# Optimization experiments

Measured on AMD Instinct MI355X. Metric: run time of the kernel, lower is better.

Reference implementation:

```python
import jax, jax.numpy as jnp
import numpy as np

VIS_DIM, VIS_NUM, EMBED, HIDDEN, VOCAB = 512, 196, 256, 512, 10000
B, T = 128, 20


def setup_inputs() -> dict:
    key = jax.random.key(0)
    ks = jax.random.split(key, 16)
    s = 0.02
    return {
        "features": jax.random.normal(ks[0], (B, VIS_NUM, VIS_DIM), jnp.float32),
        "captions": jax.random.randint(ks[1], (B, T), 0, VOCAB),
        "W_init_h": jax.random.normal(ks[2], (HIDDEN, VIS_DIM), jnp.float32) * s,
        "W_init_c": jax.random.normal(ks[3], (HIDDEN, VIS_DIM), jnp.float32) * s,
        "Wv": jax.random.normal(ks[4], (1, VIS_DIM), jnp.float32) * s,
        "bv": jnp.zeros((1,), jnp.float32),
        "Wa": jax.random.normal(ks[5], (1, HIDDEN), jnp.float32) * s,
        "ba": jnp.zeros((1,), jnp.float32),
        "embed_table": jax.random.normal(ks[6], (VOCAB, EMBED), jnp.float32) * s,
        "W_ih": jax.random.normal(ks[7], (4 * HIDDEN, VIS_DIM + EMBED), jnp.float32) * s,
        "W_hh": jax.random.normal(ks[8], (4 * HIDDEN, HIDDEN), jnp.float32) * s,
        "b_ih": jnp.zeros((4 * HIDDEN,), jnp.float32),
        "b_hh": jnp.zeros((4 * HIDDEN,), jnp.float32),
        "Wo": jax.random.normal(ks[9], (VOCAB, HIDDEN), jnp.float32) * s,
        "bo": jnp.zeros((VOCAB,), jnp.float32),
    }


def reference(features, captions, W_init_h, W_init_c, Wv, bv, Wa, ba,
              embed_table, W_ih, W_hh, b_ih, b_hh, Wo, bo):
    b, t = captions.shape
    vis_num = features.shape[1]
    # _init_hidden: sum over spatial locations of a bias-free linear, / vis_num
    h0 = jnp.sum(jnp.einsum('bnv,hv->bnh', features, W_init_h), axis=1) / vis_num  # [B,H]
    c0 = jnp.sum(jnp.einsum('bnv,hv->bnh', features, W_init_c), axis=1) / vis_num  # [B,H]
    emb = embed_table[captions]  # [B,T,E]
    # visual part of attention logits is constant across timesteps
    att_v = jnp.einsum('bnv,ov->bno', features, Wv) + bv  # [B,N,1]

    def step(carry, emb_t):
        h, c = carry
        att = att_v + (h @ Wa.T + ba)[:, None, :]          # [B,N,1]
        alpha = jax.nn.softmax(att, axis=1)                # softmax over vis_num
        ctx = jnp.sum(features * alpha, axis=1)            # [B,vis_dim]
        x = jnp.concatenate([ctx, emb_t], axis=1)          # [B,vis_dim+E]
        gates = x @ W_ih.T + b_ih + h @ W_hh.T + b_hh      # [B,4H]
        i, f, g, o = jnp.split(gates, 4, axis=1)           # torch LSTM gate order
        i, f, o = jax.nn.sigmoid(i), jax.nn.sigmoid(f), jax.nn.sigmoid(o)
        g = jnp.tanh(g)
        c = f * c + i * g
        h = o * jnp.tanh(c)
        words = h @ Wo.T + bo                              # [B,V]
        return (h, c), words

    (_, _), ws = jax.lax.scan(step, (h0, c0), jnp.swapaxes(emb, 0, 1))  # [T,B,V]
    # pack_padded_sequence (all lengths = T, batch_first) yields time-major [T*B, V]
    flat = ws.reshape(t * b, -1)
    return jax.nn.log_softmax(flat, axis=1), jax.nn.softmax(flat, axis=1)
```

## Files before the change

kernel.cpp:

```cpp
#include <hip/hip_runtime.h>

typedef unsigned short u16;
typedef unsigned int u32;
typedef unsigned long long u64;

typedef __attribute__((ext_vector_type(8))) short short8;
typedef __attribute__((ext_vector_type(4))) float float4v;

__device__ __forceinline__ float bf2f(u16 u) { return __uint_as_float(((u32)u) << 16); }
__device__ __forceinline__ u16 f2bf(float f) {
    u32 x = __float_as_uint(f);
    return (u16)((x + 0x7fffu + ((x >> 16) & 1u)) >> 16);
}
__device__ __forceinline__ float sigmoidf_(float x) { return 1.0f / (1.0f + expf(-x)); }

#define B_ 128
#define T_ 20
#define VISN 196
#define VISD 512
#define EMB 256
#define HID 512
#define VOC 10000
#define VOCP 10112
#define NBLK 64

__global__ __launch_bounds__(256) void conv_all(
    const float* __restrict__ Wih, const float* __restrict__ Whh,
    const float* __restrict__ Wo,  const float* __restrict__ Winh,
    const float* __restrict__ Winc, const float* __restrict__ bih,
    const float* __restrict__ bhh, const float* __restrict__ bo,
    u16* __restrict__ cWih, u16* __restrict__ cWhh, u16* __restrict__ cWo,
    u16* __restrict__ cWinit, u16* __restrict__ cbih, u16* __restrict__ cbhh,
    u16* __restrict__ cbo, int* __restrict__ flags) {
    const int e0 = 1572864, e1 = 2621440, e2 = 7798784, e3 = 8060928,
              e4 = 8323072, e5 = 8325120, e6 = 8327168, e7 = 8337280;
    int gid = blockIdx.x * 256 + threadIdx.x;
    if (gid < NBLK) flags[gid] = 0;
    if (gid >= e7) return;
    if (gid < e0) { cWih[gid] = f2bf(Wih[gid]); }
    else if (gid < e1) { int l = gid - e0; cWhh[l] = f2bf(Whh[l]); }
    else if (gid < e2) {
        int l = gid - e1; int row = l >> 9, col = l & 511;
        cWo[l] = (row < VOC) ? f2bf(Wo[(size_t)row * 512 + col]) : (u16)0;
    }
    else if (gid < e3) { int l = gid - e2; cWinit[l] = f2bf(Winh[l]); }
    else if (gid < e4) { int l = gid - e3; cWinit[262144 + l] = f2bf(Winc[l]); }
    else if (gid < e5) { int l = gid - e4; cbih[l] = f2bf(bih[l]); }
    else if (gid < e6) { int l = gid - e5; cbhh[l] = f2bf(bhh[l]); }
    else { int l = gid - e6; cbo[l] = (l < VOC) ? f2bf(bo[l]) : (u16)0; }
}

__global__ __launch_bounds__(256) void att_kernel(const float* __restrict__ feat,
                                                  const float* __restrict__ Wv,
                                                  float* __restrict__ alpha) {
    __shared__ float wv[512];
    __shared__ float att[VISN];
    __shared__ float red[256];
    int b = blockIdx.x, tid = threadIdx.x;
    wv[tid] = Wv[tid];
    wv[tid + 256] = Wv[tid + 256];
    __syncthreads();
    int w = tid >> 6, lane = tid & 63;
    for (int n = w; n < VISN; n += 4) {
        const float4* fp = (const float4*)(feat + ((size_t)b * VISN + n) * VISD) + lane * 2;
        float4 a = fp[0], c = fp[1];
        const float* wp = wv + lane * 8;
        float s = a.x * wp[0] + a.y * wp[1] + a.z * wp[2] + a.w * wp[3]
                + c.x * wp[4] + c.y * wp[5] + c.z * wp[6] + c.w * wp[7];
        #pragma unroll
        for (int off = 32; off; off >>= 1) s += __shfl_down(s, off);
        if (lane == 0) att[n] = s;
    }
    __syncthreads();
    float m = -1e30f;
    for (int i = tid; i < VISN; i += 256) m = fmaxf(m, att[i]);
    red[tid] = m; __syncthreads();
    for (int s = 128; s; s >>= 1) { if (tid < s) red[tid] = fmaxf(red[tid], red[tid + s]); __syncthreads(); }
    m = red[0]; __syncthreads();
    float sum = 0.f;
    for (int i = tid; i < VISN; i += 256) { float e = expf(att[i] - m); att[i] = e; sum += e; }
    red[tid] = sum; __syncthreads();
    for (int s = 128; s; s >>= 1) { if (tid < s) red[tid] += red[tid + s]; __syncthreads(); }
    float inv = 1.0f / red[0]; __syncthreads();
    for (int i = tid; i < VISN; i += 256) alpha[b * VISN + i] = att[i] * inv;
}

__global__ __launch_bounds__(256) void ctx_fbar(const float* __restrict__ feat,
                                                const float* __restrict__ alpha,
                                                u16* __restrict__ fbar_bf,
                                                u16* __restrict__ ctx_bf) {
    __shared__ float al[VISN];
    int b = blockIdx.y, tid = threadIdx.x;
    int v = blockIdx.x * 256 + tid;
    if (tid < VISN) al[tid] = alpha[b * VISN + tid];
    __syncthreads();
    float accf = 0.f, accc = 0.f;
    const float* fp = feat + (size_t)b * VISN * VISD + v;
    #pragma unroll 4
    for (int n = 0; n < VISN; n++) {
        float f = fp[(size_t)n * VISD];
        accf += f;
        accc += al[n] * f;
    }
    fbar_bf[b * VISD + v] = f2bf(accf / (float)VISN);
    ctx_bf[b * VISD + v] = f2bf(accc);
}

__global__ void gather_emb(const int* __restrict__ captions, const float* __restrict__ table,
                           u16* __restrict__ Ebf) {
    int r = blockIdx.x;
    int t = r >> 7, b = r & 127;
    int idx = captions[b * T_ + t];
    Ebf[(size_t)r * EMB + threadIdx.x] = f2bf(table[(size_t)idx * EMB + threadIdx.x]);
}

__global__ __launch_bounds__(256) void gemm_bt(const u16* __restrict__ A, int lda,
                                               const u16* __restrict__ Bm, int ldb,
                                               int M, int N, int K,
                                               const u16* __restrict__ bias0,
                                               const u16* __restrict__ bias1,
                                               const float* __restrict__ addA, int rowmask,
                                               float* __restrict__ Cf,
                                               u16* __restrict__ Cbf, int ldc, int mode) {
    __shared__ u16 As[64 * 32];
    __shared__ u16 Bs[64 * 32];
    int tid = threadIdx.x;
    int n0 = blockIdx.x * 64, m0 = blockIdx.y * 64;
    int w = tid >> 6, lane = tid & 63;
    int wm = (w & 1) * 32, wn = (w >> 1) * 32;
    int mrow = lane & 15, quad = lane >> 4;
    float4v acc[2][2] = {};
    int lr = tid >> 2;
    int lc = (tid & 3) * 8;
    for (int k0 = 0; k0 < K; k0 += 32) {
        *(uint4*)(&As[lr * 32 + lc]) = *(const uint4*)(A + (size_t)(m0 + lr) * lda + k0 + lc);
        *(uint4*)(&Bs[lr * 32 + lc]) = *(const uint4*)(Bm + (size_t)(n0 + lr) * ldb + k0 + lc);
        __syncthreads();
        short8 afrag[2], bfrag[2];
        #pragma unroll
        for (int i = 0; i < 2; i++)
            afrag[i] = *(const short8*)(&As[(wm + i * 16 + mrow) * 32 + quad * 8]);
        #pragma unroll
        for (int j = 0; j < 2; j++)
            bfrag[j] = *(const short8*)(&Bs[(wn + j * 16 + mrow) * 32 + quad * 8]);
        #pragma unroll
        for (int i = 0; i < 2; i++)
            #pragma unroll
            for (int j = 0; j < 2; j++)
                acc[i][j] = __builtin_amdgcn_mfma_f32_16x16x32_bf16(afrag[i], bfrag[j], acc[i][j], 0, 0, 0);
        __syncthreads();
    }
    #pragma unroll
    for (int i = 0; i < 2; i++) {
        #pragma unroll
        for (int j = 0; j < 2; j++) {
            #pragma unroll
            for (int r = 0; r < 4; r++) {
                int grow = m0 + wm + i * 16 + quad * 4 + r;
                int gcol = n0 + wn + j * 16 + mrow;
                float v = acc[i][j][r];
                if (bias0) v += bf2f(bias0[gcol]);
                if (bias1) v += bf2f(bias1[gcol]);
                if (addA) v += addA[(size_t)(grow & rowmask) * ldc + gcol];
                if (mode == 0) {
                    Cbf[(size_t)grow * ldc + gcol] = f2bf(v);
                } else if (mode == 1) {
                    Cf[(size_t)grow * ldc + gcol] = v;
                } else {
                    if (gcol < 512) Cbf[(size_t)grow * 512 + gcol] = f2bf(v);
                    else Cf[(size_t)grow * 512 + gcol - 512] = v;
                }
            }
        }
    }
}

__global__ __launch_bounds__(256, 1) void recurrence(
    const u16* __restrict__ Whh,
    const float* __restrict__ gbase,
    const float* __restrict__ c0,
    u16* __restrict__ h_pp,
    u16* __restrict__ h_all,
    int* __restrict__ flags) {
    __shared__ u16 Ws[64 * 520];
    int jb = blockIdx.x, tid = threadIdx.x;
    int rg = jb >> 5, cg = jb & 31;
    for (int idx = tid; idx < 64 * 64; idx += 256) {
        int lcol = idx >> 6, q8 = idx & 63;
        int grow = ((lcol >> 4) << 9) + (cg << 4) + (lcol & 15);
        *(uint4*)&Ws[lcol * 520 + q8 * 8] = *(const uint4*)&Whh[(size_t)grow * 512 + q8 * 8];
    }
    int w = tid >> 6, lane = tid & 63;
    int mrow = lane & 15, quad = lane >> 4;
    int rowA = (rg << 6) + (w << 4) + mrow;
    int rowC = (rg << 6) + (w << 4) + (quad << 2);
    int colh = (cg << 4) + mrow;
    float cst[4];
    #pragma unroll
    for (int r = 0; r < 4; r++) cst[r] = c0[(size_t)(rowC + r) * 512 + colh];
    __syncthreads();
    for (int t = 0; t < T_; t++) {
        const u16* hcur = h_pp + (t & 1) * (B_ * HID);
        u16* hnxt = h_pp + ((t + 1) & 1) * (B_ * HID);
        float gb[4][4];
        #pragma unroll
        for (int g = 0; g < 4; g++)
            #pragma unroll
            for (int r = 0; r < 4; r++)
                gb[g][r] = gbase[(size_t)(t * B_ + rowC + r) * 2048 + (g << 9) + colh];
        if (t > 0) {
            if (tid < 32) {
                while (__hip_atomic_load(&flags[(rg << 5) + tid], __ATOMIC_RELAXED,
                                         __HIP_MEMORY_SCOPE_AGENT) < t)
                    __builtin_amdgcn_s_sleep(1);
            }
            __syncthreads();
        }
        const u64* hrow = (const u64*)(hcur + (size_t)rowA * 512);
        short8 af[16];
        #pragma unroll
        for (int ks = 0; ks < 16; ks++) {
            union { u64 q[2]; short8 v; } uu;
            uu.q[0] = __hip_atomic_load(hrow + ks * 8 + quad * 2, __ATOMIC_RELAXED,
                                        __HIP_MEMORY_SCOPE_AGENT);
            uu.q[1] = __hip_atomic_load(hrow + ks * 8 + quad * 2 + 1, __ATOMIC_RELAXED,
                                        __HIP_MEMORY_SCOPE_AGENT);
            af[ks] = uu.v;
        }
        float4v acc[4] = {};
        #pragma unroll
        for (int ks = 0; ks < 16; ks++) {
            #pragma unroll
            for (int g = 0; g < 4; g++) {
                short8 bf = *(const short8*)&Ws[((g << 4) + mrow) * 520 + ks * 32 + quad * 8];
                acc[g] = __builtin_amdgcn_mfma_f32_16x16x32_bf16(af[ks], bf, acc[g], 0, 0, 0);
            }
        }
        #pragma unroll
        for (int r = 0; r < 4; r++) {
            float ig = sigmoidf_(acc[0][r] + gb[0][r]);
            float fg = sigmoidf_(acc[1][r] + gb[1][r]);
            float gg = tanhf(acc[2][r] + gb[2][r]);
            float og = sigmoidf_(acc[3][r] + gb[3][r]);
            float cn = fg * cst[r] + ig * gg;
            cst[r] = cn;
            u16 hv = f2bf(og * tanhf(cn));
            __hip_atomic_store(&hnxt[(size_t)(rowC + r) * 512 + colh], hv,
                               __ATOMIC_RELAXED, __HIP_MEMORY_SCOPE_AGENT);
            h_all[(size_t)(t * B_ + rowC + r) * 512 + colh] = hv;
        }
        asm volatile("s_waitcnt vmcnt(0)" ::: "memory");
        __syncthreads();
        if (tid == 0)
            __hip_atomic_store(&flags[jb], t + 1, __ATOMIC_RELAXED,
                               __HIP_MEMORY_SCOPE_AGENT);
    }
}

__global__ __launch_bounds__(256) void gemm128(const u16* __restrict__ A,
                                               const u16* __restrict__ Bm,
                                               const u16* __restrict__ biasbf,
                                               float* __restrict__ C) {
    __shared__ u16 As[128 * 32];
    __shared__ u16 Bs[128 * 32];
    int tid = threadIdx.x;
    int n0 = blockIdx.x * 128, m0 = blockIdx.y * 128;
    int w = tid >> 6, lane = tid & 63;
    int wm = (w & 1) * 64, wn = (w >> 1) * 64;
    int mrow = lane & 15, quad = lane >> 4;
    float4v acc[4][4] = {};
    for (int k0 = 0; k0 < 512; k0 += 32) {
        #pragma unroll
        for (int q = 0; q < 2; q++) {
            int idx = tid * 2 + q;
            int r = idx >> 2, cc = (idx & 3) * 8;
            *(uint4*)&As[r * 32 + cc] = *(const uint4*)&A[(size_t)(m0 + r) * 512 + k0 + cc];
            *(uint4*)&Bs[r * 32 + cc] = *(const uint4*)&Bm[(size_t)(n0 + r) * 512 + k0 + cc];
        }
        __syncthreads();
        short8 af[4], bfv[4];
        #pragma unroll
        for (int i = 0; i < 4; i++)
            af[i] = *(const short8*)&As[(wm + i * 16 + mrow) * 32 + quad * 8];
        #pragma unroll
        for (int jn = 0; jn < 4; jn++)
            bfv[jn] = *(const short8*)&Bs[(wn + jn * 16 + mrow) * 32 + quad * 8];
        #pragma unroll
        for (int i = 0; i < 4; i++)
            #pragma unroll
            for (int jn = 0; jn < 4; jn++)
                acc[i][jn] = __builtin_amdgcn_mfma_f32_16x16x32_bf16(af[i], bfv[jn], acc[i][jn], 0, 0, 0);
        __syncthreads();
    }
    #pragma unroll
    for (int i = 0; i < 4; i++) {
        #pragma unroll
        for (int jn = 0; jn < 4; jn++) {
            int gcol = n0 + wn + jn * 16 + mrow;
            if (gcol >= VOC) continue;
            float bias = bf2f(biasbf[gcol]);
            #pragma unroll
            for (int r = 0; r < 4; r++) {
                int grow = m0 + wm + i * 16 + quad * 4 + r;
                C[(size_t)grow * VOC + gcol] = acc[i][jn][r] + bias;
            }
        }
    }
}

__global__ __launch_bounds__(256) void softmax_out(float* __restrict__ out) {
    __shared__ float red[256];
    int r = blockIdx.x, tid = threadIdx.x;
    const size_t HALF4 = (size_t)T_ * B_ * VOC / 4;
    float4* outv = (float4*)out;
    float4* src = outv + HALF4 + (size_t)r * (VOC / 4);
    float4 lv[10];
    float m = -1e30f;
    #pragma unroll
    for (int jq = 0; jq < 10; jq++) {
        int i4 = tid + jq * 256;
        if (i4 < VOC / 4) {
            float4 v = src[i4];
            lv[jq] = v;
            m = fmaxf(m, fmaxf(fmaxf(v.x, v.y), fmaxf(v.z, v.w)));
        } else {
            lv[jq] = make_float4(-1e30f, -1e30f, -1e30f, -1e30f);
        }
    }
    red[tid] = m; __syncthreads();
    for (int s = 128; s; s >>= 1) { if (tid < s) red[tid] = fmaxf(red[tid], red[tid + s]); __syncthreads(); }
    m = red[0]; __syncthreads();
    float sum = 0.f;
    #pragma unroll
    for (int jq = 0; jq < 10; jq++)
        sum += expf(lv[jq].x - m) + expf(lv[jq].y - m) + expf(lv[jq].z - m) + expf(lv[jq].w - m);
    red[tid] = sum; __syncthreads();
    for (int s = 128; s; s >>= 1) { if (tid < s) red[tid] += red[tid + s]; __syncthreads(); }
    float logZ = m + logf(red[0]);
    float4* dls = outv + (size_t)r * (VOC / 4);
    #pragma unroll
    for (int jq = 0; jq < 10; jq++) {
        int i4 = tid + jq * 256;
        if (i4 < VOC / 4) {
            float4 v = lv[jq];
            float4 ls = make_float4(v.x - logZ, v.y - logZ, v.z - logZ, v.w - logZ);
            dls[i4] = ls;
            src[i4] = make_float4(expf(ls.x), expf(ls.y), expf(ls.z), expf(ls.w));
        }
    }
}

extern "C" void kernel_launch(void* const* d_in, const int* in_sizes, int n_in,
                              void* d_out, int out_size, void* d_ws, size_t ws_size,
                              hipStream_t stream) {
    const float* features = (const float*)d_in[0];
    const int* captions   = (const int*)d_in[1];
    const float* W_init_h = (const float*)d_in[2];
    const float* W_init_c = (const float*)d_in[3];
    const float* Wv       = (const float*)d_in[4];
    const float* embed_t  = (const float*)d_in[8];
    const float* W_ih     = (const float*)d_in[9];
    const float* W_hh     = (const float*)d_in[10];
    const float* b_ih     = (const float*)d_in[11];
    const float* b_hh     = (const float*)d_in[12];
    const float* Wo       = (const float*)d_in[13];
    const float* bo       = (const float*)d_in[14];
    float* out = (float*)d_out;

    char* base = (char*)d_ws;
    int*   flags   = (int*)(base + 0);
    float* alpha   = (float*)(base + 1024);
    u16*   fbar_bf = (u16*)(base + 103424);
    u16*   ctx_bf  = (u16*)(base + 234496);
    u16*   h_pp    = (u16*)(base + 365568);
    float* c_f32   = (float*)(base + 627712);
    float* gconst  = (float*)(base + 889856);
    u16*   Ebf     = (u16*)(base + 1938432);
    float* gbase   = (float*)(base + 3249152);
    u16*   h_all   = (u16*)(base + 24220672);
    u16*   cWih    = (u16*)(base + 26842112);
    u16*   cWhh    = (u16*)(base + 29987840);
    u16*   cWo     = (u16*)(base + 32084992);
    u16*   cWinit  = (u16*)(base + 42439680);
    u16*   cbih    = (u16*)(base + 43488256);
    u16*   cbhh    = (u16*)(base + 43492352);
    u16*   cbo     = (u16*)(base + 43496448);

    conv_all<<<32568, 256, 0, stream>>>(W_ih, W_hh, Wo, W_init_h, W_init_c,
                                        b_ih, b_hh, bo,
                                        cWih, cWhh, cWo, cWinit, cbih, cbhh, cbo, flags);
    att_kernel<<<B_, 256, 0, stream>>>(features, Wv, alpha);
    ctx_fbar<<<dim3(2, B_), 256, 0, stream>>>(features, alpha, fbar_bf, ctx_bf);
    gather_emb<<<T_ * B_, 256, 0, stream>>>(captions, embed_t, Ebf);
    gemm_bt<<<dim3(16, 2), 256, 0, stream>>>(
        fbar_bf, 512, cWinit, 512, B_, 1024, 512,
        nullptr, nullptr, nullptr, -1, c_f32, h_pp, 1024, 2);
    gemm_bt<<<dim3(32, 2), 256, 0, stream>>>(
        ctx_bf, 512, cWih, 768, B_, 2048, 512,
        cbih, cbhh, nullptr, -1, gconst, nullptr, 2048, 1);
    gemm_bt<<<dim3(32, 40), 256, 0, stream>>>(
        Ebf, 256, cWih + 512, 768, T_ * B_, 2048, 256,
        nullptr, nullptr, gconst, 127, gbase, nullptr, 2048, 1);
    recurrence<<<NBLK, 256, 0, stream>>>(cWhh, gbase, c_f32, h_pp, h_all, flags);
    gemm128<<<dim3(VOCP / 128, (T_ * B_) / 128), 256, 0, stream>>>(
        h_all, cWo, cbo, out + (size_t)T_ * B_ * VOC);
    softmax_out<<<T_ * B_, 256, 0, stream>>>(out);
}
```

Measured before the change: 614.1 us.

## Use MFMA-fragment layout for hidden state exchange and cache Whh in registers

```diff
diff --git a/kernel.cpp b/kernel.cpp
--- a/kernel.cpp
+++ b/kernel.cpp
@@ -23,6 +23,7 @@
 #define VOC 10000
 #define VOCP 10112
 #define NBLK 64
+
 
 __global__ __launch_bounds__(256) void conv_all(
     const float* __restrict__ Wih, const float* __restrict__ Whh,
@@ -35,7 +36,7 @@
     const int e0 = 1572864, e1 = 2621440, e2 = 7798784, e3 = 8060928,
               e4 = 8323072, e5 = 8325120, e6 = 8327168, e7 = 8337280;
     int gid = blockIdx.x * 256 + threadIdx.x;
-    if (gid < NBLK) flags[gid] = 0;
+    if (gid < 256) flags[gid] = 0;
     if (gid >= e7) return;
     if (gid < e0) { cWih[gid] = f2bf(Wih[gid]); }
     else if (gid < e1) { int l = gid - e0; cWhh[l] = f2bf(Whh[l]); }
@@ -167,8 +168,13 @@
                 } else if (mode == 1) {
                     Cf[(size_t)grow * ldc + gcol] = v;
                 } else {
-                    if (gcol < 512) Cbf[(size_t)grow * 512 + gcol] = f2bf(v);
-                    else Cf[(size_t)grow * 512 + gcol - 512] = v;
+                    if (gcol < 512) {
+                        size_t o = ((((size_t)(grow >> 4) * 16 + (gcol >> 5)) * 4 +
+                                     ((gcol >> 3) & 3)) * 16 + (grow & 15)) * 8 + (gcol & 7);
+                        Cbf[o] = f2bf(v);
+                    } else {
+                        Cf[(size_t)grow * 512 + gcol - 512] = v;
+                    }
                 }
             }
         }
@@ -183,6 +189,7 @@
     u16* __restrict__ h_all,
     int* __restrict__ flags) {
     __shared__ u16 Ws[64 * 520];
+    __shared__ __align__(16) u16 ex[64 * 16];
     int jb = blockIdx.x, tid = threadIdx.x;
     int rg = jb >> 5, cg = jb & 31;
     for (int idx = tid; idx < 64 * 64; idx += 256) {
@@ -192,16 +199,22 @@
     }
     int w = tid >> 6, lane = tid & 63;
     int mrow = lane & 15, quad = lane >> 4;
-    int rowA = (rg << 6) + (w << 4) + mrow;
     int rowC = (rg << 6) + (w << 4) + (quad << 2);
+    int strip = (rg << 2) + w;
     int colh = (cg << 4) + mrow;
     float cst[4];
     #pragma unroll
     for (int r = 0; r < 4; r++) cst[r] = c0[(size_t)(rowC + r) * 512 + colh];
     __syncthreads();
+    short8 bfv[16][4];
+    #pragma unroll
+    for (int ks = 0; ks < 16; ks++)
+        #pragma unroll
+        for (int g = 0; g < 4; g++)
+            bfv[ks][g] = *(const short8*)&Ws[((g << 4) + mrow) * 520 + ks * 32 + quad * 8];
     for (int t = 0; t < T_; t++) {
-        const u16* hcur = h_pp + (t & 1) * (B_ * HID);
-        u16* hnxt = h_pp + ((t + 1) & 1) * (B_ * HID);
+        const u64* hb64 = (const u64*)(h_pp + (t & 1) * 65536);
+        u16* hnxt = h_pp + ((t + 1) & 1) * 65536;
         float gb[4][4];
         #pragma unroll
         for (int g = 0; g < 4; g++)
@@ -210,32 +223,31 @@
                 gb[g][r] = gbase[(size_t)(t * B_ + rowC + r) * 2048 + (g << 9) + colh];
         if (t > 0) {
             if (tid < 32) {
-                while (__hip_atomic_load(&flags[(rg << 5) + tid], __ATOMIC_RELAXED,
+                int pj = (rg << 5) + tid;
+                int fi = ((pj & 15) << 4) + (pj >> 4);
+                while (__hip_atomic_load(&flags[fi], __ATOMIC_RELAXED,
                                          __HIP_MEMORY_SCOPE_AGENT) < t)
                     __builtin_amdgcn_s_sleep(1);
             }
             __syncthreads();
         }
-        const u64* hrow = (const u64*)(hcur + (size_t)rowA * 512);
         short8 af[16];
         #pragma unroll
         for (int ks = 0; ks < 16; ks++) {
+            int o = (((strip * 16 + ks) * 4 + quad) * 16 + mrow) * 2;
             union { u64 q[2]; short8 v; } uu;
-            uu.q[0] = __hip_atomic_load(hrow + ks * 8 + quad * 2, __ATOMIC_RELAXED,
+            uu.q[0] = __hip_atomic_load(hb64 + o, __ATOMIC_RELAXED,
                                         __HIP_MEMORY_SCOPE_AGENT);
-            uu.q[1] = __hip_atomic_load(hrow + ks * 8 + quad * 2 + 1, __ATOMIC_RELAXED,
+            uu.q[1] = __hip_atomic_load(hb64 + o + 1, __ATOMIC_RELAXED,
                                         __HIP_MEMORY_SCOPE_AGENT);
             af[ks] = uu.v;
         }
         float4v acc[4] = {};
         #pragma unroll
-        for (int ks = 0; ks < 16; ks++) {
-            #pragma unroll
-            for (int g = 0; g < 4; g++) {
-                short8 bf = *(const short8*)&Ws[((g << 4) + mrow) * 520 + ks * 32 + quad * 8];
-                acc[g] = __builtin_amdgcn_mfma_f32_16x16x32_bf16(af[ks], bf, acc[g], 0, 0, 0);
-            }
-        }
+        for (int ks = 0; ks < 16; ks++)
+            #pragma unroll
+            for (int g = 0; g < 4; g++)
+                acc[g] = __builtin_amdgcn_mfma_f32_16x16x32_bf16(af[ks], bfv[ks][g], acc[g], 0, 0, 0);
         #pragma unroll
         for (int r = 0; r < 4; r++) {
             float ig = sigmoidf_(acc[0][r] + gb[0][r]);
@@ -244,16 +256,33 @@
             float og = sigmoidf_(acc[3][r] + gb[3][r]);
             float cn = fg * cst[r] + ig * gg;
             cst[r] = cn;
-            u16 hv = f2bf(og * tanhf(cn));
-            __hip_atomic_store(&hnxt[(size_t)(rowC + r) * 512 + colh], hv,
+            ex[((w << 4) + (quad << 2) + r) * 16 + mrow] = f2bf(og * tanhf(cn));
+        }
+        __syncthreads();
+        const u32* ex32 = (const u32*)ex;
+        #pragma unroll
+        for (int h2 = 0; h2 < 2; h2++) {
+            int d = tid + h2 * 256;
+            int c = d >> 6, i = d & 63;
+            int wl = c >> 1, qs = c & 1, mw = i >> 2, ep = i & 3;
+            u32 val = ex32[((wl * 16 + mw) * 16 + qs * 8 + ep * 2) >> 1];
+            size_t o16 = ((((size_t)((rg << 2) + wl) * 16 + (cg >> 1)) * 4 +
+                          ((cg & 1) * 2 + qs)) * 16 + mw) * 8 + ep * 2;
+            __hip_atomic_store((u32*)hnxt + (o16 >> 1), val,
                                __ATOMIC_RELAXED, __HIP_MEMORY_SCOPE_AGENT);
-            h_all[(size_t)(t * B_ + rowC + r) * 512 + colh] = hv;
+        }
+        if (tid < 128) {
+            int rl = tid >> 1, hf = tid & 1;
+            uint4 v = *(const uint4*)&ex[rl * 16 + hf * 8];
+            *(uint4*)&h_all[(size_t)(t * B_ + (rg << 6) + rl) * 512 + (cg << 4) + hf * 8] = v;
         }
         asm volatile("s_waitcnt vmcnt(0)" ::: "memory");
         __syncthreads();
-        if (tid == 0)
-            __hip_atomic_store(&flags[jb], t + 1, __ATOMIC_RELAXED,
+        if (tid == 0) {
+            int fi = ((jb & 15) << 4) + (jb >> 4);
+            __hip_atomic_store(&flags[fi], t + 1, __ATOMIC_RELAXED,
                                __HIP_MEMORY_SCOPE_AGENT);
+        }
     }
 }
 
```

Measured after the change: 583.8 us. 1.05x faster.
